# Performance work log

Measured on AMD Instinct MI355X. Metric: run time of the kernel, lower is better.

The kernel has to match this reference:

```python
import jax, jax.numpy as jnp
import numpy as np

E, H, D, T, B = 768, 12, 64, 2048, 2
HID = 4 * E

def _layernorm(x, g, b, eps=1e-5):
    mu = jnp.mean(x, axis=-1, keepdims=True)
    var = jnp.mean(jnp.square(x - mu), axis=-1, keepdims=True)
    return (x - mu) * jax.lax.rsqrt(var + eps) * g + b

def setup_inputs() -> dict:
    key = jax.random.key(0)
    ks = jax.random.split(key, 8)
    s = 0.02
    return {
        "x": jax.random.normal(ks[0], (B, T, E), jnp.float32),
        "Wq": jax.random.normal(ks[1], (H, E, D), jnp.float32) * s,
        "Wk": jax.random.normal(ks[2], (H, E, D), jnp.float32) * s,
        "Wv": jax.random.normal(ks[3], (H, E, D), jnp.float32) * s,
        "W1": jax.random.normal(ks[4], (E, HID), jnp.float32) * s,
        "b1": jnp.zeros((HID,), jnp.float32),
        "W2": jax.random.normal(ks[5], (HID, E), jnp.float32) * s,
        "b2": jnp.zeros((E,), jnp.float32),
        "ln1_g": jnp.ones((E,), jnp.float32),
        "ln1_b": jnp.zeros((E,), jnp.float32),
        "ln2_g": jnp.ones((E,), jnp.float32),
        "ln2_b": jnp.zeros((E,), jnp.float32),
    }

def reference(x, Wq, Wk, Wv, W1, b1, W2, b2, ln1_g, ln1_b, ln2_g, ln2_b):
    b, t, e = x.shape
    # per-head projections (stacked): [B,H,T,D]
    q = jnp.einsum('bte,hed->bhtd', x, Wq)
    k = jnp.einsum('bte,hed->bhtd', x, Wk)
    v = jnp.einsum('bte,hed->bhtd', x, Wv)
    scores = jnp.einsum('bhtd,bhsd->bhts', q, k) / jnp.sqrt(jnp.float32(D))
    causal = jnp.tril(jnp.ones((t, t), bool))
    masked = jnp.where(causal, scores, -jnp.inf)
    p = jax.nn.softmax(masked, axis=-1)
    av = jnp.einsum('bhts,bhsd->bhtd', p, v)  # [B,H,T,D]
    attn_out = av.transpose(0, 2, 1, 3).reshape(b, t, e)  # concat heads
    y = _layernorm(x + attn_out, ln1_g, ln1_b)
    mlp = jnp.maximum(y @ W1 + b1, 0.0) @ W2 + b2
    return _layernorm(y + mlp, ln2_g, ln2_b)
```

## Files before the change

### kernel.cpp

```cpp
#include <hip/hip_runtime.h>
#include <stdint.h>

constexpr int Ee   = 768;
constexpr int Hh   = 12;
constexpr int Dd   = 64;
constexpr int Tt   = 2048;
constexpr int Bb   = 2;
constexpr int HIDc = 3072;
constexpr int MROWS = Bb * Tt;
constexpr int NQKV  = 3 * Hh * Dd;

typedef unsigned short u16;
typedef __bf16 bf16;
typedef bf16 bf16x8 __attribute__((ext_vector_type(8)));
typedef float f32x4 __attribute__((ext_vector_type(4)));
typedef float f32x16 __attribute__((ext_vector_type(16)));

__device__ __forceinline__ u16 f2bf(float f) {
  uint32_t u = __builtin_bit_cast(uint32_t, f);
  u += 0x7fffu + ((u >> 16) & 1u);
  return (u16)(u >> 16);
}

__device__ __forceinline__ float bf2f(u16 v) {
  uint32_t u = (uint32_t)v << 16;
  return __builtin_bit_cast(float, u);
}

__device__ __forceinline__ uint32_t cvt_pk_bf16(float lo, float hi) {
  uint32_t r;
  asm("v_cvt_pk_bf16_f32 %0, %1, %2" : "=v"(r) : "v"(lo), "v"(hi));
  return r;
}

__device__ __forceinline__ f32x4 mfma16(bf16x8 a, bf16x8 b, f32x4 c) {
  return __builtin_amdgcn_mfma_f32_16x16x32_bf16(a, b, c, 0, 0, 0);
}

__device__ __forceinline__ f32x16 mfma32(bf16x8 a, bf16x8 b, f32x16 c) {
  return __builtin_amdgcn_mfma_f32_32x32x16_bf16(a, b, c, 0, 0, 0);
}

#define GLOAD_LDS16(gp, lp)                                                            \
  __builtin_amdgcn_global_load_lds((const __attribute__((address_space(1))) void*)(gp),\
                                   (__attribute__((address_space(3))) void*)(lp),      \
                                   16, 0, 0)

#define KSWZ(row, byte) ((row) * 128 + ((byte) ^ (((row) & 7) << 4)))


__device__ __forceinline__ void tr_body(const float* __restrict__ ip,
                                        u16* __restrict__ op,
                                        int R, int C, int r0, int c0,
                                        float (*t)[33]) {
  const int tx = threadIdx.x & 31, ty = threadIdx.x >> 5;
#pragma unroll
  for (int i = 0; i < 4; ++i)
    t[ty * 4 + i][tx] = ip[(size_t)(r0 + ty * 4 + i) * C + c0 + tx];
  __syncthreads();
#pragma unroll
  for (int i = 0; i < 4; ++i)
    op[(size_t)(c0 + ty * 4 + i) * R + r0 + tx] = f2bf(t[tx][ty * 4 + i]);
}

__global__ __launch_bounds__(256) void prep_kernel(
    const float* __restrict__ x, u16* __restrict__ xb,
    const float* __restrict__ Wq, const float* __restrict__ Wk,
    const float* __restrict__ Wv, u16* __restrict__ wqkvt) {
  __shared__ float t[32][33];
  int bid = blockIdx.x;
  if (bid < 3072) {
    const int i = bid * 256 + threadIdx.x;
    const float4 f = *(const float4*)(x + (size_t)i * 4);
    uint2 o;
    u16* po = (u16*)&o;
    po[0] = f2bf(f.x); po[1] = f2bf(f.y); po[2] = f2bf(f.z); po[3] = f2bf(f.w);
    *(uint2*)(xb + (size_t)i * 4) = o;
    return;
  }
  bid -= 3072;
  {
    const int bx = bid & 1;
    const int rest = bid >> 1;
    const int by = rest % 24, z = rest / 24;
    const int which = z / 12, hs = z - which * 12;
    const float* W = (which == 0) ? Wq : (which == 1) ? Wk : Wv;
    tr_body(W + (size_t)hs * Ee * Dd, wqkvt + ((size_t)which * 768 + hs * 64) * Ee,
            Ee, Dd, by * 32, bx * 32, t);
  }
}

template <int EPI, int BN, int SPLITK>
__global__ __launch_bounds__(256) void gemm_bt_kernel(
    const u16* __restrict__ A, const u16* __restrict__ Bt,
    const float* __restrict__ bias,
    u16* __restrict__ out_u, u16* __restrict__ out_p,
    u16* __restrict__ qp, u16* __restrict__ kp, u16* __restrict__ vp,
    int Mdim, int Ndim, int Kdim, int gx, int gy) {
  constexpr int WN = BN / 64;
  constexpr int WM = 4 / WN;
  constexpr int MR = 128 / WM / 16;
  constexpr int ACH = 16;
  constexpr int BCH = BN / 8;
  __shared__ u16 la[2][128 * 64];
  __shared__ u16 lb[2][BN * 64];
  const int tid = threadIdx.x, lane = tid & 63, wv = tid >> 6;
  const int wm = wv / WN, wn = wv % WN;
  const int l15 = lane & 15, l4 = lane >> 4;

  const int nwg = gx * gy * SPLITK;
  const int cpx = nwg >> 3;
  const int wg = (blockIdx.x & 7) * cpx + (blockIdx.x >> 3);
  const int bx = wg % gx;
  const int byz = wg / gx;
  const int by = byz % gy;
  const int kz = byz / gy;
  const int m0 = by * 128, n0 = bx * BN;
  const int Ks = Kdim / SPLITK;
  const int kbase = kz * Ks;
  const int niter = Ks / 64;

  auto stage = [&](int it, int buf) {
    const int k0 = kbase + it * 64;
#pragma unroll
    for (int j = 0; j < ACH / 4; ++j) {
      const int cb = (wv * (ACH / 4) + j) * 64;
      const int ci = cb + lane;
      const int row = ci >> 3;
      const int kbl = ((ci & 7) * 16) ^ ((row & 7) << 4);
      GLOAD_LDS16(A + (size_t)(m0 + row) * Kdim + k0 + (kbl >> 1), la[buf] + (size_t)cb * 8);
    }
#pragma unroll
    for (int j = 0; j < BCH / 4; ++j) {
      const int cb = (wv * (BCH / 4) + j) * 64;
      const int ci = cb + lane;
      const int row = ci >> 3;
      const int kbl = ((ci & 7) * 16) ^ ((row & 7) << 4);
      GLOAD_LDS16(Bt + (size_t)(n0 + row) * Kdim + k0 + (kbl >> 1), lb[buf] + (size_t)cb * 8);
    }
  };

  f32x4 acc[MR][4] = {};
  stage(0, 0);

  for (int it = 0; it < niter; ++it) {
    __syncthreads();
    const int cur = it & 1;
    if (it + 1 < niter) stage(it + 1, cur ^ 1);
    const char* lac = (const char*)la[cur];
    const char* lbc = (const char*)lb[cur];
#pragma unroll
    for (int ks = 0; ks < 2; ++ks) {
      bf16x8 af[MR], bfr[4];
#pragma unroll
      for (int i = 0; i < MR; ++i) {
        const int row = wm * (MR * 16) + i * 16 + l15;
        af[i] = *(const bf16x8*)(lac + row * 128 +
                                 (((ks * 64 + l4 * 16)) ^ ((row & 7) << 4)));
      }
#pragma unroll
      for (int i = 0; i < 4; ++i) {
        const int row = wn * 64 + i * 16 + l15;
        bfr[i] = *(const bf16x8*)(lbc + row * 128 +
                                  (((ks * 64 + l4 * 16)) ^ ((row & 7) << 4)));
      }
      __builtin_amdgcn_s_setprio(1);
#pragma unroll
      for (int mi = 0; mi < MR; ++mi)
#pragma unroll
        for (int ni = 0; ni < 4; ++ni)
          acc[mi][ni] = mfma16(af[mi], bfr[ni], acc[mi][ni]);
      __builtin_amdgcn_s_setprio(0);
    }
  }

#pragma unroll
  for (int mi = 0; mi < MR; ++mi)
#pragma unroll
    for (int ni = 0; ni < 4; ++ni) {
      const int mb = m0 + wm * (MR * 16) + mi * 16 + l4 * 4;
      const int n = n0 + wn * 64 + ni * 16 + l15;
      if constexpr (EPI == 0) {
        const int b = mb >> 11, tb = mb & 2047;
        const int which = n / (Hh * Dd);
        const int nn = n - which * (Hh * Dd);
        const int h = nn >> 6, d = nn & 63;
        if (which == 2) {
          uint2 pw;
          pw.x = cvt_pk_bf16(acc[mi][ni][0], acc[mi][ni][1]);
          pw.y = cvt_pk_bf16(acc[mi][ni][2], acc[mi][ni][3]);
          const int tp = (tb & ~15) | ((tb & 4) << 1) | ((tb & 8) >> 1);
          *(uint2*)(vp + ((size_t)(b * Hh + h) * Dd + d) * Tt + tp) = pw;
        } else {
          u16* dst = (which == 0) ? qp : kp;
#pragma unroll
          for (int r = 0; r < 4; ++r)
            dst[((size_t)(b * Hh + h) * Tt + tb + r) * Dd + d] = f2bf(acc[mi][ni][r]);
        }
      } else if constexpr (EPI == 1) {
#pragma unroll
        for (int r = 0; r < 4; ++r) {
          float val = acc[mi][ni][r] + bias[n];
          val = fmaxf(val, 0.0f);
          out_u[(size_t)(mb + r) * Ndim + n] = f2bf(val);
        }
      } else {
#pragma unroll
        for (int r = 0; r < 4; ++r) {
          float val = acc[mi][ni][r];
          if (kz == 0) val += bias[n];
          out_p[(size_t)kz * Mdim * Ndim + (size_t)(mb + r) * Ndim + n] = f2bf(val);
        }
      }
    }
}

__global__ __launch_bounds__(256) void attn_kernel(const u16* __restrict__ q,
                                                   const u16* __restrict__ k,
                                                   const u16* __restrict__ vtg,
                                                   u16* __restrict__ Pb,
                                                   float* __restrict__ Lb,
                                                   const float* __restrict__ W1,
                                                   u16* __restrict__ w1t,
                                                   const float* __restrict__ W2,
                                                   u16* __restrict__ w2t) {
  __shared__ u16 kl[2][64 * 64];
  __shared__ u16 vt[2][64 * 64];
  const int bid = blockIdx.x;
  if (bid >= 960) {
    float (*tt)[33] = (float(*)[33])kl;
    int b2 = bid - 960;
    if (b2 < 2304) {
      const int bx = b2 % 96, by = b2 / 96;
      tr_body(W1, w1t, Ee, HIDc, by * 32, bx * 32, tt);
    } else {
      b2 -= 2304;
      const int bx = b2 % 24, by = b2 / 24;
      tr_body(W2, w2t, HIDc, Ee, by * 32, bx * 32, tt);
    }
    return;
  }
  const int tid = threadIdx.x, lane = tid & 63, w = tid >> 6;
  const int l31 = lane & 31, hi = lane >> 5;
  const int x8 = bid & 7, r3 = bid >> 3;
  const int g = r3 % 3, u = r3 / 3;
  int q128, c, nt;
  if (u < 4)       { q128 = 15; c = u; nt = 8; }
  else if (u < 16) { const int v = u - 4;  q128 = 14 - v / 3; c = v % 3; nt = 8; }
  else if (u < 24) { const int v = u - 16; q128 = 10 - v / 2; c = v % 2; nt = 8; }
  else if (u < 28) { q128 = 6 - (u - 24); c = 0; nt = 8; }
  else             { const int v = u - 28; const int row = v >> 2, col = v & 3;
                     nt = 6 - 2 * row; q128 = 14 - row - 4 * col; c = 3 - col; }
  const int ts0 = c * 8;
  const int bh = g * 8 + x8;
  const int wq = 2 * q128 + (w >> 1);
  const int tg = q128 * 128 + (w >> 1) * 64 + (w & 1) * 32 + l31;
  constexpr float SC = 0.18033688f;

  const u16* kgb = k + (size_t)bh * Tt * Dd;
  const u16* vgb = vtg + (size_t)bh * Dd * Tt;

  bf16x8 qf[4];
#pragma unroll
  for (int kt = 0; kt < 4; ++kt)
    qf[kt] = *(const bf16x8*)(q + ((size_t)bh * Tt + tg) * Dd + kt * 16 + hi * 8);

  {
    const int sb0 = ts0 * 64;
#pragma unroll
    for (int jj = 0; jj < 2; ++jj) {
      const int cb = (w * 2 + jj) * 64;
      const int ci = cb + lane;
      const int row = ci >> 3;
      const int sb = ((ci & 7) * 16) ^ ((row & 7) << 4);
      GLOAD_LDS16(kgb + (size_t)(sb0 + row) * Dd + (sb >> 1), kl[0] + (size_t)cb * 8);
      GLOAD_LDS16(vgb + (size_t)row * Tt + sb0 + (sb >> 1), vt[0] + (size_t)cb * 8);
    }
  }

  f32x16 oacc0 = {}, oacc1 = {};
  float lrun = 0.f;

  for (int jt = 0; jt < nt; ++jt) {
    __syncthreads();
    const int cur = jt & 1;
    if (jt + 1 < nt) {
      const int s0n = (ts0 + jt + 1) * 64;
#pragma unroll
      for (int jj = 0; jj < 2; ++jj) {
        const int cb = (w * 2 + jj) * 64;
        const int ci = cb + lane;
        const int row = ci >> 3;
        const int sb = ((ci & 7) * 16) ^ ((row & 7) << 4);
        GLOAD_LDS16(kgb + (size_t)(s0n + row) * Dd + (sb >> 1), kl[cur ^ 1] + (size_t)cb * 8);
        GLOAD_LDS16(vgb + (size_t)row * Tt + s0n + (sb >> 1), vt[cur ^ 1] + (size_t)cb * 8);
      }
    }
    const int tile = ts0 + jt;
    if (tile <= wq) {
      const u16* klc = kl[cur];
      const u16* vtc = vt[cur];

      f32x16 sacc0 = {}, sacc1 = {};
      __builtin_amdgcn_s_setprio(1);
#pragma unroll
      for (int kt = 0; kt < 4; ++kt) {
        const int b0 = kt * 32 + hi * 16;
        const bf16x8 kf0 = *(const bf16x8*)((const char*)klc + KSWZ(l31, b0));
        const bf16x8 kf1 = *(const bf16x8*)((const char*)klc + KSWZ(32 + l31, b0));
        sacc0 = mfma32(kf0, qf[kt], sacc0);
        sacc1 = mfma32(kf1, qf[kt], sacc1);
      }
      __builtin_amdgcn_s_setprio(0);

      const bool diag = (tile == wq);
      bf16x8 pf[4];
      float rs = 0.f;
#pragma unroll
      for (int sh = 0; sh < 2; ++sh) {
        const f32x16 sa = sh ? sacc1 : sacc0;
#pragma unroll
        for (int kt2 = 0; kt2 < 2; ++kt2) {
          float p8[8];
#pragma unroll
          for (int o = 0; o < 8; ++o) {
            const int r = kt2 * 8 + o;
            float e = __builtin_amdgcn_exp2f(sa[r] * SC);
            if (diag) {
              const int sg = tile * 64 + sh * 32 + kt2 * 16 + (o & 3) + 8 * (o >> 2) + 4 * hi;
              e = (sg > tg) ? 0.f : e;
            }
            p8[o] = e;
            rs += e;
          }
          uint4 uu;
          uu.x = cvt_pk_bf16(p8[0], p8[1]);
          uu.y = cvt_pk_bf16(p8[2], p8[3]);
          uu.z = cvt_pk_bf16(p8[4], p8[5]);
          uu.w = cvt_pk_bf16(p8[6], p8[7]);
          pf[sh * 2 + kt2] = __builtin_bit_cast(bf16x8, uu);
        }
      }
      lrun += rs;

      __builtin_amdgcn_s_setprio(1);
#pragma unroll
      for (int ks = 0; ks < 4; ++ks) {
        const int b0 = ks * 32 + hi * 16;
        const bf16x8 vf0 = *(const bf16x8*)((const char*)vtc + KSWZ(l31, b0));
        const bf16x8 vf1 = *(const bf16x8*)((const char*)vtc + KSWZ(32 + l31, b0));
        oacc0 = mfma32(vf0, pf[ks], oacc0);
        oacc1 = mfma32(vf1, pf[ks], oacc1);
      }
      __builtin_amdgcn_s_setprio(0);
    }
  }

  const float lt = lrun + __shfl_xor(lrun, 32);
  const int b = bh / Hh, h = bh - (bh / Hh) * Hh;
  u16* orow = Pb + (size_t)c * MROWS * Ee + ((size_t)b * Tt + tg) * Ee + h * Dd;
#pragma unroll
  for (int dt = 0; dt < 2; ++dt) {
    const f32x16 oa = dt ? oacc1 : oacc0;
#pragma unroll
    for (int kq = 0; kq < 4; ++kq) {
      uint2 pw;
      pw.x = cvt_pk_bf16(oa[4 * kq + 0], oa[4 * kq + 1]);
      pw.y = cvt_pk_bf16(oa[4 * kq + 2], oa[4 * kq + 3]);
      *(uint2*)(orow + dt * 32 + 8 * kq + 4 * hi) = pw;
    }
  }
  if (hi == 0)
    Lb[(size_t)c * MROWS * 12 + ((size_t)b * Tt + tg) * 12 + h] = lt;
}

__global__ __launch_bounds__(256) void ln1_kernel(const u16* __restrict__ xb,
                                                  const u16* __restrict__ P,
                                                  const float* __restrict__ L,
                                                  const float* __restrict__ g,
                                                  const float* __restrict__ beta,
                                                  u16* __restrict__ ybout) {
  const int w = threadIdx.x >> 6, lane = threadIdx.x & 63;
  const int m = blockIdx.x * 4 + w;
  const int t = m & (Tt - 1);
  float inv = 0.f;
  if (lane < 12) {
    float s = L[(size_t)m * 12 + lane];
    if (t >= 512)  s += L[(size_t)(1 * MROWS + m) * 12 + lane];
    if (t >= 1024) s += L[(size_t)(2 * MROWS + m) * 12 + lane];
    if (t >= 1536) s += L[(size_t)(3 * MROWS + m) * 12 + lane];
    inv = 1.0f / s;
  }
  float vbuf[12];
  float s = 0.f, ss = 0.f;
#pragma unroll
  for (int j = 0; j < 3; ++j) {
    const int e = j * 256 + lane * 4;
    const float ih = __shfl(inv, 4 * j + (lane >> 4));
    float o[4];
    {
      const uint2 p0 = *(const uint2*)(P + (size_t)m * Ee + e);
      const u16* pp = (const u16*)&p0;
#pragma unroll
      for (int r = 0; r < 4; ++r) o[r] = bf2f(pp[r]);
    }
    if (t >= 512) {
      const uint2 p1 = *(const uint2*)(P + (size_t)(1 * MROWS + m) * Ee + e);
      const u16* pp = (const u16*)&p1;
#pragma unroll
      for (int r = 0; r < 4; ++r) o[r] += bf2f(pp[r]);
    }
    if (t >= 1024) {
      const uint2 p2 = *(const uint2*)(P + (size_t)(2 * MROWS + m) * Ee + e);
      const u16* pp = (const u16*)&p2;
#pragma unroll
      for (int r = 0; r < 4; ++r) o[r] += bf2f(pp[r]);
    }
    if (t >= 1536) {
      const uint2 p3 = *(const uint2*)(P + (size_t)(3 * MROWS + m) * Ee + e);
      const u16* pp = (const u16*)&p3;
#pragma unroll
      for (int r = 0; r < 4; ++r) o[r] += bf2f(pp[r]);
    }
    const uint2 xv = *(const uint2*)(xb + (size_t)m * Ee + e);
    const u16* xp = (const u16*)&xv;
#pragma unroll
    for (int r = 0; r < 4; ++r) {
      const float tv = bf2f(xp[r]) + o[r] * ih;
      vbuf[j * 4 + r] = tv;
      s += tv;
      ss += tv * tv;
    }
  }
#pragma unroll
  for (int off = 1; off < 64; off <<= 1) {
    s += __shfl_xor(s, off);
    ss += __shfl_xor(ss, off);
  }
  const float mu = s / Ee;
  const float var = ss / Ee - mu * mu;
  const float rinv = rsqrtf(var + 1e-5f);
#pragma unroll
  for (int j = 0; j < 3; ++j) {
    const int e = j * 256 + lane * 4;
    const float4 gv = *(const float4*)(g + e);
    const float4 bv = *(const float4*)(beta + e);
    const float t0 = (vbuf[j * 4 + 0] - mu) * rinv * gv.x + bv.x;
    const float t1 = (vbuf[j * 4 + 1] - mu) * rinv * gv.y + bv.y;
    const float t2 = (vbuf[j * 4 + 2] - mu) * rinv * gv.z + bv.z;
    const float t3 = (vbuf[j * 4 + 3] - mu) * rinv * gv.w + bv.w;
    uint2 pw;
    pw.x = cvt_pk_bf16(t0, t1);
    pw.y = cvt_pk_bf16(t2, t3);
    *(uint2*)(ybout + (size_t)m * Ee + e) = pw;
  }
}

__global__ __launch_bounds__(256) void ln2_kernel(const u16* __restrict__ a,
                                                  const u16* __restrict__ mlp,
                                                  const float* __restrict__ g,
                                                  const float* __restrict__ beta,
                                                  float* __restrict__ yout) {
  const int w = threadIdx.x >> 6, lane = threadIdx.x & 63;
  const int m = blockIdx.x * 4 + w;
  float vbuf[12];
  float s = 0.f, ss = 0.f;
#pragma unroll
  for (int j = 0; j < 3; ++j) {
    const int e = j * 256 + lane * 4;
    float o[4];
    {
      const uint2 p0 = *(const uint2*)(a + (size_t)m * Ee + e);
      const u16* pp = (const u16*)&p0;
#pragma unroll
      for (int r = 0; r < 4; ++r) o[r] = bf2f(pp[r]);
    }
#pragma unroll
    for (int kz = 0; kz < 2; ++kz) {
      const uint2 p1 = *(const uint2*)(mlp + (size_t)(kz * MROWS + m) * Ee + e);
      const u16* pp = (const u16*)&p1;
#pragma unroll
      for (int r = 0; r < 4; ++r) o[r] += bf2f(pp[r]);
    }
#pragma unroll
    for (int r = 0; r < 4; ++r) {
      vbuf[j * 4 + r] = o[r];
      s += o[r];
      ss += o[r] * o[r];
    }
  }
#pragma unroll
  for (int off = 1; off < 64; off <<= 1) {
    s += __shfl_xor(s, off);
    ss += __shfl_xor(ss, off);
  }
  const float mu = s / Ee;
  const float var = ss / Ee - mu * mu;
  const float rinv = rsqrtf(var + 1e-5f);
#pragma unroll
  for (int j = 0; j < 3; ++j) {
    const int e = j * 256 + lane * 4;
    const float4 gv = *(const float4*)(g + e);
    const float4 bv = *(const float4*)(beta + e);
    float4 ov;
    ov.x = (vbuf[j * 4 + 0] - mu) * rinv * gv.x + bv.x;
    ov.y = (vbuf[j * 4 + 1] - mu) * rinv * gv.y + bv.y;
    ov.z = (vbuf[j * 4 + 2] - mu) * rinv * gv.z + bv.z;
    ov.w = (vbuf[j * 4 + 3] - mu) * rinv * gv.w + bv.w;
    *(float4*)(yout + (size_t)m * Ee + e) = ov;
  }
}

extern "C" void kernel_launch(void* const* d_in, const int* in_sizes, int n_in,
                              void* d_out, int out_size, void* d_ws, size_t ws_size,
                              hipStream_t stream) {
  const float* x  = (const float*)d_in[0];
  const float* Wq = (const float*)d_in[1];
  const float* Wk = (const float*)d_in[2];
  const float* Wv = (const float*)d_in[3];
  const float* W1 = (const float*)d_in[4];
  const float* b1 = (const float*)d_in[5];
  const float* W2 = (const float*)d_in[6];
  const float* b2 = (const float*)d_in[7];
  const float* g1 = (const float*)d_in[8];
  const float* be1 = (const float*)d_in[9];
  const float* g2 = (const float*)d_in[10];
  const float* be2 = (const float*)d_in[11];
  float* out = (float*)d_out;

  char* ws = (char*)d_ws;
  size_t off = 0;
  auto alloc = [&](size_t bytes) -> char* {
    char* p = ws + off;
    off += (bytes + 255) & ~(size_t)255;
    return p;
  };
  u16* xb    = (u16*)alloc((size_t)MROWS * Ee * 2);
  u16* wqkvt = (u16*)alloc((size_t)NQKV * Ee * 2);
  u16* w1t   = (u16*)alloc((size_t)HIDc * Ee * 2);
  u16* w2t   = (u16*)alloc((size_t)Ee * HIDc * 2);
  u16* qb    = (u16*)alloc((size_t)Bb * Hh * Tt * Dd * 2);
  u16* kb    = (u16*)alloc((size_t)Bb * Hh * Tt * Dd * 2);
  u16* vtb   = (u16*)alloc((size_t)Bb * Hh * Tt * Dd * 2);
  u16* yb     = (u16*)alloc((size_t)MROWS * Ee * 2);
  float* Lb   = (float*)alloc((size_t)4 * MROWS * 12 * 4);
  char* big = alloc((size_t)MROWS * HIDc * 2 + (size_t)2 * MROWS * Ee * 2);
  u16* Pb    = (u16*)big;
  u16* hbuf  = (u16*)big;
  u16* mlp   = (u16*)(big + (size_t)MROWS * HIDc * 2);
  (void)ws_size;

  prep_kernel<<<4800, 256, 0, stream>>>(x, xb, Wq, Wk, Wv, wqkvt);

  gemm_bt_kernel<0, 64, 1><<<36 * 32, 256, 0, stream>>>(
      xb, wqkvt, nullptr, nullptr, nullptr, qb, kb, vtb, MROWS, NQKV, Ee, 36, 32);

  attn_kernel<<<960 + 4608, 256, 0, stream>>>(qb, kb, vtb, Pb, Lb, W1, w1t, W2, w2t);

  ln1_kernel<<<MROWS / 4, 256, 0, stream>>>(xb, Pb, Lb, g1, be1, yb);

  gemm_bt_kernel<1, 64, 1><<<48 * 32, 256, 0, stream>>>(
      yb, w1t, b1, hbuf, nullptr, nullptr, nullptr, nullptr, MROWS, HIDc, Ee, 48, 32);
  gemm_bt_kernel<2, 64, 2><<<12 * 32 * 2, 256, 0, stream>>>(
      hbuf, w2t, b2, nullptr, mlp, nullptr, nullptr, nullptr, MROWS, Ee, HIDc, 12, 32);

  ln2_kernel<<<MROWS / 4, 256, 0, stream>>>(yb, mlp, g2, be2, out);
}
```

Before: 138.2 us.

## Replace W1 GEMM with 256x256 tiled, 8-wave ping-pong pipelined kernel

Adds a dedicated GEMM kernel for the first MLP projection that uses 256x256 output tiles, 512 threads, and double-buffered LDS staged in halves with direct global-to-LDS loads. Loads for upcoming K-tiles are interleaved with MFMA quadrants, using explicit vmcnt waits and s_setprio. The goal is higher MFMA utilisation and more data reuse than the prior 64-tile generic GEMM. It launches only 192 blocks, which may underfill the GPU, and it uses a large LDS footprint.

```diff
diff --git a/kernel.cpp b/kernel.cpp
--- a/kernel.cpp
+++ b/kernel.cpp
@@ -211,6 +211,137 @@
           if (kz == 0) val += bias[n];
           out_p[(size_t)kz * Mdim * Ndim + (size_t)(mb + r) * Ndim + n] = f2bf(val);
         }
+      }
+    }
+}
+
+__global__ __launch_bounds__(512) void gemm8p_kernel(
+    const u16* __restrict__ A, const u16* __restrict__ Bt,
+    const float* __restrict__ bias, u16* __restrict__ out_u) {
+  constexpr int KD = 768, ND = HIDc;
+  constexpr int NT = KD / 64;
+  constexpr int NI = NT / 2;
+  __shared__ u16 la[2][256 * 64];
+  __shared__ u16 lb[2][256 * 64];
+  const int tid = threadIdx.x, lane = tid & 63, wid = tid >> 6;
+  const int wr = wid >> 2, wc = wid & 3;
+  const int l15 = lane & 15, l4 = lane >> 4;
+  const int bx = blockIdx.x % (ND / 256), by = blockIdx.x / (ND / 256);
+  const int m0 = by * 256, n0 = bx * 256;
+
+  auto stageHalf = [&](int which, int kt, int h, int buf) {
+    const int k0 = kt * 64;
+#pragma unroll
+    for (int j = 0; j < 2; ++j) {
+      const int cb = j * 512 + wid * 64;
+      const int ci = cb + lane;
+      const int rl = ci >> 3;
+      int r, boff;
+      if (which == 0) {
+        r = (rl & 63) | ((rl >> 6) << 7) | (h << 6);
+        boff = ((cb & 511) << 4) | ((cb >> 9) << 14) | (h << 13);
+      } else {
+        r = (rl & 31) | ((rl >> 5) << 6) | (h << 5);
+        boff = ((cb & 255) << 4) | ((cb >> 8) << 13) | (h << 12);
+      }
+      const int slot = ci & 7;
+      const int kb = (slot * 16) ^ ((r & 7) << 4);
+      if (which == 0)
+        GLOAD_LDS16(A + (size_t)(m0 + r) * KD + k0 + (kb >> 1),
+                    (u16*)((char*)la[buf] + boff));
+      else
+        GLOAD_LDS16(Bt + (size_t)(n0 + r) * KD + k0 + (kb >> 1),
+                    (u16*)((char*)lb[buf] + boff));
+    }
+  };
+
+  f32x4 acc[8][4] = {};
+  bf16x8 afq[4][2], bfq[2][2];
+
+#define READ_A(lac, qm)                                                        \
+  { _Pragma("unroll") for (int mf = 0; mf < 4; ++mf)                           \
+      _Pragma("unroll") for (int kh = 0; kh < 2; ++kh) {                       \
+        const int row = wr * 128 + (qm) * 64 + mf * 16 + l15;                  \
+        afq[mf][kh] = *(const bf16x8*)((lac) + row * 128 +                     \
+                       ((kh * 64 + l4 * 16) ^ ((row & 7) << 4)));              \
+      } }
+#define READ_B(lbc, qn)                                                        \
+  { _Pragma("unroll") for (int nf = 0; nf < 2; ++nf)                           \
+      _Pragma("unroll") for (int kh = 0; kh < 2; ++kh) {                       \
+        const int row = wc * 64 + (qn) * 32 + nf * 16 + l15;                   \
+        bfq[nf][kh] = *(const bf16x8*)((lbc) + row * 128 +                     \
+                       ((kh * 64 + l4 * 16) ^ ((row & 7) << 4)));              \
+      } }
+#define DO_MFMA(qm, qn)                                                        \
+  __builtin_amdgcn_s_setprio(1);                                               \
+  _Pragma("unroll") for (int kh = 0; kh < 2; ++kh)                             \
+    _Pragma("unroll") for (int mf = 0; mf < 4; ++mf)                           \
+      _Pragma("unroll") for (int nf = 0; nf < 2; ++nf)                         \
+        acc[(qm) * 4 + mf][(qn) * 2 + nf] =                                    \
+            mfma16(afq[mf][kh], bfq[nf][kh], acc[(qm) * 4 + mf][(qn) * 2 + nf]); \
+  __builtin_amdgcn_s_setprio(0);
+#define VMW4 asm volatile("s_waitcnt vmcnt(4)" ::: "memory")
+#define VMW0 asm volatile("s_waitcnt vmcnt(0)" ::: "memory")
+#define BARR __builtin_amdgcn_s_barrier()
+
+  stageHalf(0, 0, 0, 0);
+  stageHalf(1, 0, 1, 0);
+  stageHalf(0, 0, 1, 0);
+  stageHalf(1, 0, 0, 0);
+  stageHalf(0, 1, 0, 1);
+  stageHalf(1, 1, 1, 1);
+
+  const char* l0a = (const char*)la[0];
+  const char* l0b = (const char*)lb[0];
+  const char* l1a = (const char*)la[1];
+  const char* l1b = (const char*)lb[1];
+
+  for (int i = 0; i < NI; ++i) {
+    const int tB = 2 * i + 1, tC = 2 * i + 2, tD = 2 * i + 3;
+    VMW4; BARR;
+    stageHalf(0, tB, 1, 1);
+    READ_A(l0a, 0); READ_B(l0b, 0); DO_MFMA(0, 0);
+    BARR;
+    stageHalf(1, tB, 0, 1);
+    READ_B(l0b, 1); DO_MFMA(0, 1);
+    BARR;
+    if (tC < NT) stageHalf(0, tC, 0, 0);
+    READ_A(l0a, 1); DO_MFMA(1, 1);
+    BARR;
+    if (tC < NT) stageHalf(1, tC, 1, 0);
+    READ_B(l0b, 0); DO_MFMA(1, 0);
+    if (i + 1 < NI) { VMW4; } else { VMW0; }
+    BARR;
+    if (tC < NT) stageHalf(0, tC, 1, 0);
+    READ_A(l1a, 0); READ_B(l1b, 0); DO_MFMA(0, 0);
+    BARR;
+    if (tC < NT) stageHalf(1, tC, 0, 0);
+    READ_B(l1b, 1); DO_MFMA(0, 1);
+    BARR;
+    if (tD < NT) stageHalf(0, tD, 0, 1);
+    READ_A(l1a, 1); DO_MFMA(1, 1);
+    BARR;
+    if (tD < NT) stageHalf(1, tD, 1, 1);
+    READ_B(l1b, 0); DO_MFMA(1, 0);
+  }
+#undef READ_A
+#undef READ_B
+#undef DO_MFMA
+#undef VMW4
+#undef VMW0
+#undef BARR
+
+#pragma unroll
+  for (int mi = 0; mi < 8; ++mi)
+#pragma unroll
+    for (int ni = 0; ni < 4; ++ni) {
+      const int mb = m0 + wr * 128 + mi * 16 + l4 * 4;
+      const int n = n0 + wc * 64 + ni * 16 + l15;
+#pragma unroll
+      for (int r = 0; r < 4; ++r) {
+        float val = acc[mi][ni][r] + bias[n];
+        val = fmaxf(val, 0.0f);
+        out_u[(size_t)(mb + r) * ND + n] = f2bf(val);
       }
     }
 }
@@ -559,8 +690,7 @@
 
   ln1_kernel<<<MROWS / 4, 256, 0, stream>>>(xb, Pb, Lb, g1, be1, yb);
 
-  gemm_bt_kernel<1, 64, 1><<<48 * 32, 256, 0, stream>>>(
-      yb, w1t, b1, hbuf, nullptr, nullptr, nullptr, nullptr, MROWS, HIDc, Ee, 48, 32);
+  gemm8p_kernel<<<16 * 12, 512, 0, stream>>>(yb, w1t, b1, hbuf);
   gemm_bt_kernel<2, 64, 2><<<12 * 32 * 2, 256, 0, stream>>>(
       hbuf, w2t, b2, nullptr, mlp, nullptr, nullptr, nullptr, MROWS, Ee, HIDc, 12, 32);
 
```

New measurement: 141.8 us. 2.6% more time.
